# Kernel optimization log

Measured on AMD Instinct MI355X. Metric: run time of the kernel, lower is better.

The kernel has to match this reference:

```python
import jax, jax.numpy as jnp
import numpy as np

N_NODES = 10000
N_EDGES = 320000
F_NODE = 16
NUM_BESSEL = 8
M = 32           # env_embed_multiplicity
LAT = 128        # latent dimension
R_MAX = 5.0
P_CUT = 6.0      # polynomial cutoff order
AVG_NEIGH = 32.0
SQRT3 = 1.7320508075688772
SQRT2 = 1.4142135623730951


def _mlp(x, weights):
    # nequip ScalarMLPFunction: linear layers with 1/sqrt(fan_in) norm, silu between layers
    h = x
    n = len(weights)
    for i, W in enumerate(weights):
        h = h @ W * (1.0 / np.sqrt(W.shape[0]))
        if i < n - 1:
            h = jax.nn.silu(h)
    return h


def _weight_channels(Y, w):
    # MakeWeightedChannels: Y [E,4] = (0e | 1e), w [E,M,2] per-irrep weights -> [E,M,4]
    return jnp.concatenate([w[..., 0:1] * Y[:, None, 0:1],
                            w[..., 1:2] * Y[:, None, 1:4]], axis=-1)


def setup_inputs():
    key = jax.random.key(0)
    ks = jax.random.split(key, 16)

    def w(k, i, o):
        return jax.random.normal(k, (i, o), jnp.float32)

    two_body_in = 2 * F_NODE + NUM_BESSEL  # 40
    return {
        "coordinates": jax.random.uniform(ks[0], (N_NODES, 3), jnp.float32),
        "node_attrs": jax.random.uniform(ks[1], (N_NODES, F_NODE), jnp.float32),
        "edge_index": jax.random.randint(ks[2], (2, N_EDGES), 0, N_NODES),
        "W2b0": w(ks[3], two_body_in, 64),
        "W2b1": w(ks[4], 64, 128),
        "W2b2": w(ks[5], 128, LAT),
        "Wenv0": w(ks[6], LAT, 4 * M),       # initial-edge embed + env weights (2 irreps each)
        "Wlat0": w(ks[7], LAT + 2 * M, 128),
        "Wlat1": w(ks[8], 128, LAT),
        "Ws0": w(ks[9], 2 * M, M),            # e3nn Linear, scalar block (2 paths)
        "Wv0": w(ks[10], 3 * M, M),           # e3nn Linear, vector block (3 paths)
        "Wenv1": w(ks[11], LAT, 2 * M),
        "Wfin0": w(ks[12], LAT + 2 * M, 128),
        "Wfin1": w(ks[13], 128, LAT),
    }


def reference(coordinates, node_attrs, edge_index, W2b0, W2b1, W2b2, Wenv0,
              Wlat0, Wlat1, Ws0, Wv0, Wenv1, Wfin0, Wfin1):
    sender, center = edge_index[0], edge_index[1]
    vec = coordinates[center] - coordinates[sender]            # [E,3]
    r = jnp.sqrt(jnp.sum(vec * vec, axis=-1) + 1e-12)          # [E]
    u = r / R_MAX
    p = P_CUT
    fcut = (1.0 - (p + 1.0) * (p + 2.0) / 2.0 * u**p
            + p * (p + 2.0) * u**(p + 1.0)
            - p * (p + 1.0) / 2.0 * u**(p + 2.0))
    fcut = jnp.where(u < 1.0, fcut, 0.0)
    n = jnp.arange(1, NUM_BESSEL + 1, dtype=jnp.float32)
    bessel = np.sqrt(2.0 / R_MAX) * jnp.sin(n * jnp.pi * u[:, None]) / r[:, None]
    edge_feats = bessel * fcut[:, None]                        # [E,8]
    unit = vec / r[:, None]
    Y = jnp.concatenate([jnp.ones_like(r)[:, None], SQRT3 * unit], axis=-1)  # [E,4] component-normalized SH

    inv_sqrt_n = 1.0 / np.sqrt(AVG_NEIGH)
    E = r.shape[0]

    # two-body latent (layer 0)
    lat_in = jnp.concatenate([node_attrs[center], node_attrs[sender], edge_feats], -1)
    lat = _mlp(lat_in, (W2b0, W2b1, W2b2)) * fcut[:, None]     # [E,LAT]
    w_all = lat @ Wenv0 * (1.0 / np.sqrt(LAT))                 # [E,4M]
    w_edge = w_all[:, :2 * M].reshape(E, M, 2)
    w_env = w_all[:, 2 * M:].reshape(E, M, 2)
    feat = _weight_channels(Y, w_edge)                         # [E,M,4] initial edge embed
    env = jax.ops.segment_sum(_weight_channels(Y, w_env), center, num_segments=N_NODES)
    env = env[center] * inv_sqrt_n                             # [E,M,4]

    fs, fv = feat[..., 0], feat[..., 1:]
    es, ev = env[..., 0], env[..., 1:]
    # layer-0 tensor product instruction list (uuu, no weights)
    p0 = fs * es                               # 0e x 0e -> 0e
    p1 = jnp.sum(fv * ev, -1) / SQRT3          # 1e x 1e -> 0e
    p2 = fs[..., None] * ev                    # 0e x 1e -> 1e
    p3 = fv * es[..., None]                    # 1e x 0e -> 1e
    p4 = jnp.cross(fv, ev) / SQRT2             # 1e x 1e -> 1e
    scal0 = jnp.concatenate([p0, p1], -1)      # [E,2M] scalar outs (n_scalar_outs=2)
    # per-layer e3nn Linear
    s_mix = scal0 @ Ws0 * (1.0 / np.sqrt(2 * M))                         # [E,M]
    v_mix = jnp.einsum('eic,io->eoc', jnp.concatenate([p2, p3, p4], 1), Wv0) * (1.0 / np.sqrt(3 * M))  # [E,M,3]

    # latent resnet update (update param 0 -> sigmoid = 0.5)
    alpha = 0.5
    c_old = 1.0 / np.sqrt(alpha * alpha + 1.0)
    c_new = alpha * c_old
    new_lat = _mlp(jnp.concatenate([lat, scal0], -1), (Wlat0, Wlat1)) * fcut[:, None]
    lat = c_old * lat + c_new * new_lat

    # layer 1 env embedding + tensor product (last layer -> scalars only)
    w_env1 = (lat @ Wenv1 * (1.0 / np.sqrt(LAT))).reshape(E, M, 2)
    env1 = jax.ops.segment_sum(_weight_channels(Y, w_env1), center, num_segments=N_NODES)
    env1 = env1[center] * inv_sqrt_n
    q0 = s_mix * env1[..., 0]
    q1 = jnp.sum(v_mix * env1[..., 1:], -1) / SQRT3
    scal1 = jnp.concatenate([q0, q1], -1)      # [E,2M]

    new_lat = _mlp(jnp.concatenate([lat, scal1], -1), (Wfin0, Wfin1)) * fcut[:, None]
    lat = c_old * lat + c_new * new_lat

    node_out = jax.ops.segment_sum(lat, center, num_segments=N_NODES) * inv_sqrt_n
    return node_out
```

## Files before the change

kernel.cpp:

```cpp
#include <hip/hip_runtime.h>
#include <hip/hip_bf16.h>
#include <math.h>

typedef __hip_bfloat16 bf16;
typedef __attribute__((ext_vector_type(8))) short short8;
typedef __attribute__((ext_vector_type(4))) float floatx4;

#define AMODE_PLAIN  0
#define AMODE_CONCAT 2
#define EPI_SPLIT    1
#define EPI_STORE    2
#define EPI_FCUT     3
#define EPI_RESID    4

#define INV_SQRT_N 0.17677669529663687f
#define INV_SQRT3  0.5773502691896258f
#define INV_SQRT2  0.7071067811865476f
#define C_OLD      0.8944271909999159f
#define C_NEW      0.4472135954999579f
#define PI_F       3.14159265358979323846f
#define SQRT3_F    1.7320508075688772f
#define BESSEL_PREF 0.6324555320336759f

__device__ __forceinline__ float b2f(bf16 x) { return __bfloat162float(x); }
__device__ __forceinline__ bf16  f2b(float x) { return __float2bfloat16(x); }
__device__ __forceinline__ unsigned short f2bu(float x) {
  bf16 h = f2b(x); unsigned short u; __builtin_memcpy(&u, &h, 2); return u;
}
__device__ __forceinline__ float silu_f(float v) { return v / (1.f + __expf(-v)); }
__device__ __forceinline__ floatx4 mfma16(short8 a, short8 b, floatx4 c) {
  return __builtin_amdgcn_mfma_f32_16x16x32_bf16(a, b, c, 0, 0, 0);
}

__global__ __launch_bounds__(256) void k_deg(
    const int* __restrict__ eidx, int E, int* __restrict__ deg) {
  int e = blockIdx.x * 256 + threadIdx.x;
  if (e < E) atomicAdd(&deg[eidx[E + e]], 1);
}

__global__ __launch_bounds__(1024) void k_scan(
    const int* __restrict__ deg, int N,
    int* __restrict__ rowptr, int* __restrict__ cursor) {
  __shared__ int part[1024];
  int t = threadIdx.x;
  int C = (N + 1023) / 1024;
  int base = t * C;
  int s = 0;
  for (int i = 0; i < C; ++i) { int idx = base + i; if (idx < N) s += deg[idx]; }
  part[t] = s;
  __syncthreads();
  for (int off = 1; off < 1024; off <<= 1) {
    int v = (t >= off) ? part[t - off] : 0;
    __syncthreads();
    part[t] += v;
    __syncthreads();
  }
  int excl = (t == 0) ? 0 : part[t - 1];
  for (int i = 0; i < C; ++i) {
    int idx = base + i;
    if (idx < N) { rowptr[idx] = excl; cursor[idx] = excl; excl += deg[idx]; }
  }
  if (t == 0) rowptr[N] = part[1023];
}

__global__ __launch_bounds__(256) void k_fill(
    const int* __restrict__ eidx, int E, int* __restrict__ cursor,
    int* __restrict__ eord, int* __restrict__ cent) {
  int e = blockIdx.x * 256 + threadIdx.x;
  if (e >= E) return;
  int c = eidx[E + e];
  int slot = atomicAdd(&cursor[c], 1);
  eord[slot] = e;
  cent[slot] = c;
}

__global__ __launch_bounds__(256) void k_geom(
    const float* __restrict__ coords, const float* __restrict__ nattr,
    const int* __restrict__ eidx, const int* __restrict__ eord, int E,
    float* __restrict__ fcut, float* __restrict__ Yb, bf16* __restrict__ a40) {
  int j = blockIdx.x * 256 + threadIdx.x;
  if (j >= E) return;
  int e = eord[j];
  int s = eidx[e], c = eidx[E + e];
  float dx = coords[c*3+0] - coords[s*3+0];
  float dy = coords[c*3+1] - coords[s*3+1];
  float dz = coords[c*3+2] - coords[s*3+2];
  float r = sqrtf(dx*dx + dy*dy + dz*dz + 1e-12f);
  float u = r * 0.2f;
  float u3 = u*u*u;
  float u6 = u3*u3, u7 = u6*u, u8 = u7*u;
  float fc = 1.f - 28.f*u6 + 48.f*u7 - 21.f*u8;
  fc = (u < 1.f) ? fc : 0.f;
  float inv_r = 1.f / r;
  fcut[j] = fc;
  Yb[j*4+0] = 1.f;
  Yb[j*4+1] = SQRT3_F * dx * inv_r;
  Yb[j*4+2] = SQRT3_F * dy * inv_r;
  Yb[j*4+3] = SQRT3_F * dz * inv_r;
  bf16* row = a40 + (long)j * 40;
  #pragma unroll
  for (int i = 0; i < 16; ++i) row[i]      = f2b(nattr[(long)c*16 + i]);
  #pragma unroll
  for (int i = 0; i < 16; ++i) row[16 + i] = f2b(nattr[(long)s*16 + i]);
  float pref = BESSEL_PREF * inv_r * fc;
  #pragma unroll
  for (int n = 1; n <= 8; ++n)
    row[32 + n - 1] = f2b(pref * sinf((float)n * PI_F * u));
}

__device__ __forceinline__ void wp(const float* W, unsigned short* Wt,
                                   int K, int NOUT, int t) {
  int n = t / K, k = t % K;
  Wt[n * K + k] = f2bu(W[k * NOUT + n]);
}

__global__ __launch_bounds__(256) void k_wprep_all(
    const float* W2b0, const float* W2b1, const float* W2b2,
    const float* Wenv0, const float* Wlat0, const float* Wlat1,
    const float* Wenv1, const float* Wfin0, const float* Wfin1,
    const float* Ws0, const float* Wv0,
    unsigned short* W2b0t, unsigned short* W2b1t, unsigned short* W2b2t,
    unsigned short* Wenv0t, unsigned short* Wlat0t, unsigned short* Wlat1t,
    unsigned short* Wenv1t, unsigned short* Wfin0t, unsigned short* Wfin1t,
    unsigned short* Wmixt) {
  int t = blockIdx.x * 256 + threadIdx.x;
  if (t < 8192)  { wp(W2b1,  W2b1t,  64, 128, t); return; } t -= 8192;
  if (t < 16384) { wp(W2b2,  W2b2t, 128, 128, t); return; } t -= 16384;
  if (t < 16384) { wp(Wenv0, Wenv0t,128, 128, t); return; } t -= 16384;
  if (t < 24576) { wp(Wlat0, Wlat0t,192, 128, t); return; } t -= 24576;
  if (t < 16384) { wp(Wlat1, Wlat1t,128, 128, t); return; } t -= 16384;
  if (t < 8192)  { wp(Wenv1, Wenv1t,128,  64, t); return; } t -= 8192;
  if (t < 24576) { wp(Wfin0, Wfin0t,192, 128, t); return; } t -= 24576;
  if (t < 16384) { wp(Wfin1, Wfin1t,128, 128, t); return; } t -= 16384;
  if (t < 2560)  { wp(W2b0,  W2b0t,  40,  64, t); return; } t -= 2560;
  if (t < 5120) {
    int o = t / 160, k = t % 160;
    float v = (k < 64) ? Ws0[k * 32 + o] : Wv0[(k - 64) * 32 + o];
    Wmixt[o * 160 + k] = f2bu(v);
  }
}

__global__ __launch_bounds__(256) void k_envg(
    const bf16* __restrict__ wenv, const float* __restrict__ Yb,
    const int* __restrict__ rowptr, int N, float* __restrict__ env) {
  int t = blockIdx.x * 256 + threadIdx.x;
  if (t >= N * 32) return;
  int n = t >> 5, m = t & 31;
  int j0 = rowptr[n], j1 = rowptr[n + 1];
  float a0 = 0.f, a1 = 0.f, a2 = 0.f, a3 = 0.f;
  for (int j = j0; j < j1; ++j) {
    float w0 = b2f(wenv[(long)j*64 + 2*m]);
    float w1 = b2f(wenv[(long)j*64 + 2*m + 1]);
    float4 y = *reinterpret_cast<const float4*>(&Yb[(long)j*4]);
    a0 += w0;
    a1 += w1 * y.y;
    a2 += w1 * y.z;
    a3 += w1 * y.w;
  }
  *reinterpret_cast<float4*>(&env[(long)n*128 + m*4]) = make_float4(a0, a1, a2, a3);
}

__global__ __launch_bounds__(256) void k_nodeg(
    const bf16* __restrict__ lat, const int* __restrict__ rowptr,
    int N, float* __restrict__ out) {
  int t = blockIdx.x * 256 + threadIdx.x;
  if (t >= N * 128) return;
  int n = t >> 7, j = t & 127;
  int j0 = rowptr[n], j1 = rowptr[n + 1];
  float s = 0.f;
  for (int q = j0; q < j1; ++q)
    s += b2f(lat[(long)q*128 + j]);
  out[t] = s * INV_SQRT_N;
}

__global__ __launch_bounds__(256) void mgemm40(
    const bf16* __restrict__ A, const unsigned short* __restrict__ Wt,
    bf16* __restrict__ out, float scale, int E) {
  __shared__ __align__(16) unsigned short As[64 * 72];
  __shared__ __align__(16) unsigned short Bs[64 * 72];
  int tid = threadIdx.x;
  int lane = tid & 63, w = tid >> 6;
  int nl = lane & 15, quad = lane >> 4;
  long e0 = (long)blockIdx.x * 64;

  for (int i = tid; i < 512; i += 256) {
    int e = i >> 3, h = i & 7;
    short8 v = {0,0,0,0,0,0,0,0};
    long eg = e0 + e;
    if (h < 5 && eg < E) v = *(const short8*)(A + eg * 40 + h * 8);
    *(short8*)&As[e * 72 + h * 8] = v;
  }
  for (int i = tid; i < 512; i += 256) {
    int n = i >> 3, h = i & 7;
    short8 v = {0,0,0,0,0,0,0,0};
    if (h < 5) v = *(const short8*)(Wt + n * 40 + h * 8);
    *(short8*)&Bs[n * 72 + h * 8] = v;
  }
  __syncthreads();

  floatx4 acc[4];
  #pragma unroll
  for (int i = 0; i < 4; ++i) acc[i] = (floatx4){0.f,0.f,0.f,0.f};
  #pragma unroll
  for (int ks = 0; ks < 2; ++ks) {
    short8 af[4];
    #pragma unroll
    for (int et = 0; et < 4; ++et)
      af[et] = *(const short8*)&As[(et*16 + nl) * 72 + ks*32 + quad*8];
    short8 bv = *(const short8*)&Bs[(w*16 + nl) * 72 + ks*32 + quad*8];
    #pragma unroll
    for (int et = 0; et < 4; ++et) acc[et] = mfma16(af[et], bv, acc[et]);
  }
  #pragma unroll
  for (int et = 0; et < 4; ++et)
    #pragma unroll
    for (int r = 0; r < 4; ++r) {
      long eg = e0 + et*16 + quad*4 + r;
      if (eg >= E) continue;
      out[eg * 64 + w*16 + nl] = f2b(silu_f(acc[et][r] * scale));
    }
}

template<int K, int NOUT, int EPI>
__global__ __launch_bounds__(256) void mgemm(
    const bf16* __restrict__ A, const unsigned short* __restrict__ Wt,
    bf16* __restrict__ out1, bf16* __restrict__ out2, float scale, int E) {
  constexpr int KP = 40;
  constexpr int CT = NOUT / 64;
  __shared__ __align__(16) unsigned short As[64 * KP];
  __shared__ __align__(16) unsigned short Bs[NOUT * KP];
  int tid = threadIdx.x;
  int lane = tid & 63, w = tid >> 6;
  int nl = lane & 15, quad = lane >> 4;
  long e0 = (long)blockIdx.x * 64;

  floatx4 acc[4][CT];
  #pragma unroll
  for (int i = 0; i < 4; ++i)
    #pragma unroll
    for (int j = 0; j < CT; ++j) acc[i][j] = (floatx4){0.f,0.f,0.f,0.f};

  int ae = tid & 63, akh = tid >> 6;
  long aeg = e0 + ae;

  for (int k0 = 0; k0 < K; k0 += 32) {
    if (k0) __syncthreads();
    {
      short8 v = {0,0,0,0,0,0,0,0};
      if (aeg < E) v = *(const short8*)(A + aeg * (long)K + k0 + akh * 8);
      *(short8*)&As[ae * KP + akh * 8] = v;
    }
    if constexpr (NOUT == 128) {
      int j = tid >> 1, h = tid & 1;
      const short8* s = (const short8*)(Wt + (long)j * K + k0 + h * 16);
      *(short8*)&Bs[j * KP + h * 16]     = s[0];
      *(short8*)&Bs[j * KP + h * 16 + 8] = s[1];
    } else {
      int j = tid >> 2, h = tid & 3;
      *(short8*)&Bs[j * KP + h * 8] =
          *(const short8*)(Wt + (long)j * K + k0 + h * 8);
    }
    __syncthreads();
    short8 af[4], bv[CT];
    #pragma unroll
    for (int et = 0; et < 4; ++et)
      af[et] = *(const short8*)&As[(et*16 + nl) * KP + quad * 8];
    #pragma unroll
    for (int ct = 0; ct < CT; ++ct)
      bv[ct] = *(const short8*)&Bs[(w*CT*16 + ct*16 + nl) * KP + quad * 8];
    #pragma unroll
    for (int et = 0; et < 4; ++et)
      #pragma unroll
      for (int ct = 0; ct < CT; ++ct)
        acc[et][ct] = mfma16(af[et], bv[ct], acc[et][ct]);
  }

  #pragma unroll
  for (int et = 0; et < 4; ++et)
    #pragma unroll
    for (int ct = 0; ct < CT; ++ct)
      #pragma unroll
      for (int r = 0; r < 4; ++r) {
        long eg = e0 + et*16 + quad*4 + r;
        if (eg >= E) continue;
        int col = w*CT*16 + ct*16 + nl;
        float v = acc[et][ct][r] * scale;
        if constexpr (EPI == EPI_SPLIT) {
          if (col < 64) out1[eg * 64 + col] = f2b(v);
          else          out2[eg * 64 + (col - 64)] = f2b(v);
        } else {
          out1[eg * NOUT + col] = f2b(v);
        }
      }
}

template<int K, int AMODE, int EPI>
__global__ __launch_bounds__(256) void mfused(
    const bf16* __restrict__ A, const bf16* __restrict__ A2,
    const unsigned short* __restrict__ W0t, const unsigned short* __restrict__ W1t,
    bf16* __restrict__ outb, const float* __restrict__ fcut,
    float scale0, float scale1, int E) {
  constexpr int KP = 40, HP = 136;
  __shared__ __align__(16) unsigned short As[64 * KP];
  __shared__ __align__(16) unsigned short Bs[128 * KP];
  __shared__ __align__(16) unsigned short Hs[64 * HP];
  int tid = threadIdx.x;
  int lane = tid & 63, w = tid >> 6;
  int nl = lane & 15, quad = lane >> 4;
  long e0 = (long)blockIdx.x * 64;

  floatx4 acc[4][2];
  #pragma unroll
  for (int i = 0; i < 4; ++i)
    #pragma unroll
    for (int j = 0; j < 2; ++j) acc[i][j] = (floatx4){0.f,0.f,0.f,0.f};

  int ae = tid & 63, akh = tid >> 6;
  long aeg = e0 + ae;
  int bj = tid >> 1, bh = tid & 1;

  for (int k0 = 0; k0 < K; k0 += 32) {
    if (k0) __syncthreads();
    {
      int kk = k0 + akh * 8;
      short8 v = {0,0,0,0,0,0,0,0};
      if (aeg < E) {
        const bf16* src;
        if constexpr (AMODE == AMODE_PLAIN) src = A + aeg * (long)K + kk;
        else src = (kk < 128) ? (A + aeg * 128 + kk) : (A2 + aeg * 64 + (kk - 128));
        v = *(const short8*)src;
      }
      *(short8*)&As[ae * KP + akh * 8] = v;
    }
    {
      const short8* s = (const short8*)(W0t + (long)bj * K + k0 + bh * 16);
      *(short8*)&Bs[bj * KP + bh * 16]     = s[0];
      *(short8*)&Bs[bj * KP + bh * 16 + 8] = s[1];
    }
    __syncthreads();
    short8 af[4], bv[2];
    #pragma unroll
    for (int et = 0; et < 4; ++et)
      af[et] = *(const short8*)&As[(et*16 + nl) * KP + quad * 8];
    #pragma unroll
    for (int ct = 0; ct < 2; ++ct)
      bv[ct] = *(const short8*)&Bs[(w*32 + ct*16 + nl) * KP + quad * 8];
    #pragma unroll
    for (int et = 0; et < 4; ++et)
      #pragma unroll
      for (int ct = 0; ct < 2; ++ct)
        acc[et][ct] = mfma16(af[et], bv[ct], acc[et][ct]);
  }

  #pragma unroll
  for (int et = 0; et < 4; ++et)
    #pragma unroll
    for (int ct = 0; ct < 2; ++ct)
      #pragma unroll
      for (int r = 0; r < 4; ++r) {
        int el = et*16 + quad*4 + r;
        int h  = w*32 + ct*16 + nl;
        Hs[el * HP + h] = f2bu(silu_f(acc[et][ct][r] * scale0));
      }
  #pragma unroll
  for (int i = 0; i < 4; ++i)
    #pragma unroll
    for (int j = 0; j < 2; ++j) acc[i][j] = (floatx4){0.f,0.f,0.f,0.f};

  for (int k0 = 0; k0 < 128; k0 += 32) {
    __syncthreads();
    {
      const short8* s = (const short8*)(W1t + (long)bj * 128 + k0 + bh * 16);
      *(short8*)&Bs[bj * KP + bh * 16]     = s[0];
      *(short8*)&Bs[bj * KP + bh * 16 + 8] = s[1];
    }
    __syncthreads();
    short8 af[4], bv[2];
    #pragma unroll
    for (int et = 0; et < 4; ++et)
      af[et] = *(const short8*)&Hs[(et*16 + nl) * HP + k0 + quad * 8];
    #pragma unroll
    for (int ct = 0; ct < 2; ++ct)
      bv[ct] = *(const short8*)&Bs[(w*32 + ct*16 + nl) * KP + quad * 8];
    #pragma unroll
    for (int et = 0; et < 4; ++et)
      #pragma unroll
      for (int ct = 0; ct < 2; ++ct)
        acc[et][ct] = mfma16(af[et], bv[ct], acc[et][ct]);
  }

  #pragma unroll
  for (int et = 0; et < 4; ++et)
    #pragma unroll
    for (int ct = 0; ct < 2; ++ct)
      #pragma unroll
      for (int r = 0; r < 4; ++r) {
        long eg = e0 + et*16 + quad*4 + r;
        if (eg >= E) continue;
        int col = w*32 + ct*16 + nl;
        float fc = fcut[eg];
        float v = acc[et][ct][r] * scale1 * fc;
        if constexpr (EPI == EPI_FCUT) {
          outb[eg * 128 + col] = f2b(v);
        } else {
          long idx = eg * 128 + col;
          outb[idx] = f2b(C_OLD * b2f(outb[idx]) + C_NEW * v);
        }
      }
}

__global__ __launch_bounds__(256) void k_prod(
    const bf16* __restrict__ wedge, const float* __restrict__ env,
    const float* __restrict__ Yb, const int* __restrict__ cent, int E,
    bf16* __restrict__ scal) {
  long t = (long)blockIdx.x * 256 + threadIdx.x;
  if (t >= (long)E * 32) return;
  long e = t >> 5;
  int m = (int)(t & 31);
  int c = cent[e];
  float w0 = b2f(wedge[e*64 + 2*m]), w1 = b2f(wedge[e*64 + 2*m + 1]);
  const float* ep = env + (long)c*128 + m*4;
  float es  = ep[0] * INV_SQRT_N;
  float evx = ep[1] * INV_SQRT_N, evy = ep[2] * INV_SQRT_N, evz = ep[3] * INV_SQRT_N;
  float y1 = Yb[e*4+1], y2 = Yb[e*4+2], y3 = Yb[e*4+3];
  float fvx = w1*y1, fvy = w1*y2, fvz = w1*y3;
  scal[e*64 + m]      = f2b(w0 * es);
  scal[e*64 + 32 + m] = f2b((fvx*evx + fvy*evy + fvz*evz) * INV_SQRT3);
}

__global__ __launch_bounds__(256) void k_mix2(
    const bf16* __restrict__ wedge, const float* __restrict__ env,
    const float* __restrict__ env1, const float* __restrict__ Yb,
    const int* __restrict__ cent, const unsigned short* __restrict__ Wm,
    int E, bf16* __restrict__ scal) {
  constexpr int PP = 360;
  constexpr int RP = 132;
  __shared__ __align__(16) unsigned char SB[64 * PP * 2];
  __shared__ __align__(16) unsigned short Wl[32 * 160];
  unsigned short* P = (unsigned short*)SB;
  float* R = (float*)SB;
  int tid = threadIdx.x;
  int lane = tid & 63, w = tid >> 6;
  int nl = lane & 15, quad = lane >> 4;
  long e0 = (long)blockIdx.x * 64;

  for (int i = tid; i < 640; i += 256)
    *(short8*)&Wl[i * 8] = *(const short8*)(Wm + i * 8);

  int m = tid & 31;
  #pragma unroll
  for (int it = 0; it < 8; ++it) {
    int el = (tid >> 5) + it * 8;
    long e = e0 + el;
    if (e < E) {
      int c = cent[e];
      float w0 = b2f(wedge[e*64 + 2*m]), w1 = b2f(wedge[e*64 + 2*m + 1]);
      float4 ev4 = *(const float4*)(env + (long)c*128 + m*4);
      float4 y   = *(const float4*)(Yb + e*4);
      float es  = ev4.x * INV_SQRT_N;
      float evx = ev4.y * INV_SQRT_N, evy = ev4.z * INV_SQRT_N, evz = ev4.w * INV_SQRT_N;
      float fvx = w1*y.y, fvy = w1*y.z, fvz = w1*y.w;
      unsigned short* p = P + el * PP;
      p[m]       = f2bu(w0 * es);
      p[32 + m]  = f2bu((fvx*evx + fvy*evy + fvz*evz) * INV_SQRT3);
      p[64 + m]  = f2bu(w0 * evx);
      p[96 + m]  = f2bu(fvx * es);
      p[128 + m] = f2bu((fvy*evz - fvz*evy) * INV_SQRT2);
      p[160 + m] = f2bu(w0 * evy);
      p[192 + m] = f2bu(fvy * es);
      p[224 + m] = f2bu((fvz*evx - fvx*evz) * INV_SQRT2);
      p[256 + m] = f2bu(w0 * evz);
      p[288 + m] = f2bu(fvz * es);
      p[320 + m] = f2bu((fvx*evy - fvy*evx) * INV_SQRT2);
    } else {
      unsigned short* p = P + el * PP;
      #pragma unroll
      for (int q = 0; q < 11; ++q) p[q*32 + m] = 0;
    }
  }
  __syncthreads();

  floatx4 acc[4][2];
  #pragma unroll
  for (int i = 0; i < 4; ++i)
    #pragma unroll
    for (int j = 0; j < 2; ++j) acc[i][j] = (floatx4){0.f,0.f,0.f,0.f};
  int pbase  = (w == 0) ? 0 : 64 + (w - 1) * 96;
  int wkbase = (w == 0) ? 0 : 64;
  int ksteps = (w == 0) ? 2 : 3;
  for (int ks = 0; ks < ksteps; ++ks) {
    short8 af[4], bv[2];
    #pragma unroll
    for (int et = 0; et < 4; ++et)
      af[et] = *(const short8*)&P[(et*16 + nl) * PP + pbase + ks*32 + quad*8];
    #pragma unroll
    for (int ct = 0; ct < 2; ++ct)
      bv[ct] = *(const short8*)&Wl[(ct*16 + nl) * 160 + wkbase + ks*32 + quad*8];
    #pragma unroll
    for (int et = 0; et < 4; ++et)
      #pragma unroll
      for (int ct = 0; ct < 2; ++ct)
        acc[et][ct] = mfma16(af[et], bv[ct], acc[et][ct]);
  }
  __syncthreads();

  #pragma unroll
  for (int et = 0; et < 4; ++et)
    #pragma unroll
    for (int ct = 0; ct < 2; ++ct)
      #pragma unroll
      for (int r = 0; r < 4; ++r) {
        int el = et*16 + quad*4 + r;
        R[el * RP + w*32 + ct*16 + nl] = acc[et][ct][r];
      }
  __syncthreads();

  #pragma unroll
  for (int it = 0; it < 8; ++it) {
    int el = (tid >> 5) + it * 8;
    long e = e0 + el;
    if (e >= E) continue;
    int o = m;
    int c = cent[e];
    float4 e1 = *(const float4*)(env1 + (long)c*128 + o*4);
    float sr = R[el * RP + o];
    float vx = R[el * RP + 32 + o];
    float vy = R[el * RP + 64 + o];
    float vz = R[el * RP + 96 + o];
    float q0 = sr * 0.125f * (e1.x * INV_SQRT_N);
    float q1 = (vx*e1.y + vy*e1.z + vz*e1.w) *
               (0.10206207261596577f * INV_SQRT_N * INV_SQRT3);
    scal[e*64 + o]      = f2b(q0);
    scal[e*64 + 32 + o] = f2b(q1);
  }
}

extern "C" void kernel_launch(void* const* d_in, const int* in_sizes, int n_in,
                              void* d_out, int out_size, void* d_ws, size_t ws_size,
                              hipStream_t stream) {
  const float* coords = (const float*)d_in[0];
  const float* nattr  = (const float*)d_in[1];
  const int*   eidx   = (const int*)d_in[2];
  const float* W2b0   = (const float*)d_in[3];
  const float* W2b1   = (const float*)d_in[4];
  const float* W2b2   = (const float*)d_in[5];
  const float* Wenv0  = (const float*)d_in[6];
  const float* Wlat0  = (const float*)d_in[7];
  const float* Wlat1  = (const float*)d_in[8];
  const float* Ws0    = (const float*)d_in[9];
  const float* Wv0    = (const float*)d_in[10];
  const float* Wenv1  = (const float*)d_in[11];
  const float* Wfin0  = (const float*)d_in[12];
  const float* Wfin1  = (const float*)d_in[13];
  float* out = (float*)d_out;
  int E = in_sizes[2] / 2;
  int N = in_sizes[0] / 3;

  float* fcut   = (float*)d_ws;
  float* Yb     = fcut + (size_t)E;
  float* env    = Yb + (size_t)E*4;
  float* env1   = env + (size_t)N*128;
  int*   deg    = (int*)(env1 + (size_t)N*128);
  int*   rowptr = deg + N;
  int*   cursor = rowptr + (N + 8);
  int*   eord   = cursor + N;
  int*   cent   = eord + E;
  bf16*  b64    = (bf16*)(cent + E);
  bf16*  lat    = b64 + (size_t)E*64;
  bf16*  S      = lat + (size_t)E*128;
  unsigned short* W2b1t  = (unsigned short*)(S + (size_t)E*64);
  unsigned short* W2b2t  = W2b1t + 128*64;
  unsigned short* Wenv0t = W2b2t + 128*128;
  unsigned short* Wlat0t = Wenv0t + 128*128;
  unsigned short* Wlat1t = Wlat0t + 128*192;
  unsigned short* Wenv1t = Wlat1t + 128*128;
  unsigned short* Wfin0t = Wenv1t + 64*128;
  unsigned short* Wfin1t = Wfin0t + 128*192;
  unsigned short* W2b0t  = Wfin1t + 128*128;
  unsigned short* Wmixt  = W2b0t + 64*40;

  hipMemsetAsync(deg, 0, (size_t)N * sizeof(int), stream);

  dim3 blk(256);
  const float s40  = 0.15811388300841897f;
  const float s64  = 0.125f;
  const float s128 = 0.08838834764831845f;
  const float s192 = 0.07216878364870323f;
  int gB = (E + 63) / 64;
  int gE = (E + 255) / 256;

  k_deg<<<gE, blk, 0, stream>>>(eidx, E, deg);
  k_scan<<<1, 1024, 0, stream>>>(deg, N, rowptr, cursor);
  k_fill<<<gE, blk, 0, stream>>>(eidx, E, cursor, eord, cent);
  k_geom<<<gE, blk, 0, stream>>>(coords, nattr, eidx, eord, E, fcut, Yb, S );
  k_wprep_all<<<dim3(542), blk, 0, stream>>>(
      W2b0, W2b1, W2b2, Wenv0, Wlat0, Wlat1, Wenv1, Wfin0, Wfin1, Ws0, Wv0,
      W2b0t, W2b1t, W2b2t, Wenv0t, Wlat0t, Wlat1t, Wenv1t, Wfin0t, Wfin1t, Wmixt);

  mgemm40<<<gB, blk, 0, stream>>>(S , W2b0t, b64, s40, E);
  mfused<64,AMODE_PLAIN,EPI_FCUT><<<gB, blk, 0, stream>>>(
      b64, nullptr, W2b1t, W2b2t, lat, fcut, s64, s128, E);

  mgemm<128,128,EPI_SPLIT><<<gB, blk, 0, stream>>>(
      lat, Wenv0t, b64, S , s128, E);

  k_envg<<<dim3((N*32 + 255) / 256), blk, 0, stream>>>(
      S , Yb, rowptr, N, env);

  k_prod<<<dim3((int)(((long)E*32 + 255) / 256)), blk, 0, stream>>>(
      b64, env, Yb, cent, E, S );

  mfused<192,AMODE_CONCAT,EPI_RESID><<<gB, blk, 0, stream>>>(
      lat, S , Wlat0t, Wlat1t, lat, fcut, s192, s128, E);

  mgemm<128,64,EPI_STORE><<<gB, blk, 0, stream>>>(
      lat, Wenv1t, S , nullptr, s128, E);

  k_envg<<<dim3((N*32 + 255) / 256), blk, 0, stream>>>(
      S , Yb, rowptr, N, env1);

  k_mix2<<<gB, blk, 0, stream>>>(
      b64, env, env1, Yb, cent, Wmixt, E, S );

  mfused<192,AMODE_CONCAT,EPI_RESID><<<gB, blk, 0, stream>>>(
      lat, S , Wfin0t, Wfin1t, lat, fcut, s192, s128, E);

  k_nodeg<<<dim3((N*128 + 255) / 256), blk, 0, stream>>>(
      lat, rowptr, N, out);
}
```

Measured before the change: 724.1 us.

## Fuse two-body MLP into one kernel and load GEMM operands directly from global

The first two-body layer (K=40, padded to 64) is merged with the next two layers into a single kernel, so the intermediate 64-wide activation stays in LDS and is no longer written to and re-read from global memory. The generic GEMM and fused-MLP kernels stop staging A and weight tiles through shared memory with barriers. MFMA fragments are now read straight from global memory, relying on cache for weight reuse. Padding the geometry row to 64 adds a little extra write traffic, and the direct global fragment loads may be less coalesced than the old staged loads.

```diff
diff --git a/kernel.cpp b/kernel.cpp
--- a/kernel.cpp
+++ b/kernel.cpp
@@ -3,6 +3,7 @@
 #include <math.h>
 
 typedef __hip_bfloat16 bf16;
+typedef unsigned short us;
 typedef __attribute__((ext_vector_type(8))) short short8;
 typedef __attribute__((ext_vector_type(4))) float floatx4;
 
@@ -24,12 +25,15 @@
 
 __device__ __forceinline__ float b2f(bf16 x) { return __bfloat162float(x); }
 __device__ __forceinline__ bf16  f2b(float x) { return __float2bfloat16(x); }
-__device__ __forceinline__ unsigned short f2bu(float x) {
-  bf16 h = f2b(x); unsigned short u; __builtin_memcpy(&u, &h, 2); return u;
+__device__ __forceinline__ us f2bu(float x) {
+  bf16 h = f2b(x); us u; __builtin_memcpy(&u, &h, 2); return u;
 }
 __device__ __forceinline__ float silu_f(float v) { return v / (1.f + __expf(-v)); }
 __device__ __forceinline__ floatx4 mfma16(short8 a, short8 b, floatx4 c) {
   return __builtin_amdgcn_mfma_f32_16x16x32_bf16(a, b, c, 0, 0, 0);
+}
+__device__ __forceinline__ short8 ld8(const void* p) {
+  return *reinterpret_cast<const short8*>(p);
 }
 
 __global__ __launch_bounds__(256) void k_deg(
@@ -77,7 +81,7 @@
 __global__ __launch_bounds__(256) void k_geom(
     const float* __restrict__ coords, const float* __restrict__ nattr,
     const int* __restrict__ eidx, const int* __restrict__ eord, int E,
-    float* __restrict__ fcut, float* __restrict__ Yb, bf16* __restrict__ a40) {
+    float* __restrict__ fcut, float* __restrict__ Yb, bf16* __restrict__ a64) {
   int j = blockIdx.x * 256 + threadIdx.x;
   if (j >= E) return;
   int e = eord[j];
@@ -97,7 +101,7 @@
   Yb[j*4+1] = SQRT3_F * dx * inv_r;
   Yb[j*4+2] = SQRT3_F * dy * inv_r;
   Yb[j*4+3] = SQRT3_F * dz * inv_r;
-  bf16* row = a40 + (long)j * 40;
+  bf16* row = a64 + (long)j * 64;
   #pragma unroll
   for (int i = 0; i < 16; ++i) row[i]      = f2b(nattr[(long)c*16 + i]);
   #pragma unroll
@@ -106,10 +110,11 @@
   #pragma unroll
   for (int n = 1; n <= 8; ++n)
     row[32 + n - 1] = f2b(pref * sinf((float)n * PI_F * u));
-}
-
-__device__ __forceinline__ void wp(const float* W, unsigned short* Wt,
-                                   int K, int NOUT, int t) {
+  #pragma unroll
+  for (int i = 40; i < 64; ++i) row[i] = f2b(0.f);
+}
+
+__device__ __forceinline__ void wp(const float* W, us* Wt, int K, int NOUT, int t) {
   int n = t / K, k = t % K;
   Wt[n * K + k] = f2bu(W[k * NOUT + n]);
 }
@@ -119,10 +124,8 @@
     const float* Wenv0, const float* Wlat0, const float* Wlat1,
     const float* Wenv1, const float* Wfin0, const float* Wfin1,
     const float* Ws0, const float* Wv0,
-    unsigned short* W2b0t, unsigned short* W2b1t, unsigned short* W2b2t,
-    unsigned short* Wenv0t, unsigned short* Wlat0t, unsigned short* Wlat1t,
-    unsigned short* Wenv1t, unsigned short* Wfin0t, unsigned short* Wfin1t,
-    unsigned short* Wmixt) {
+    us* W2b0p, us* W2b1t, us* W2b2t, us* Wenv0t, us* Wlat0t, us* Wlat1t,
+    us* Wenv1t, us* Wfin0t, us* Wfin1t, us* Wmixt) {
   int t = blockIdx.x * 256 + threadIdx.x;
   if (t < 8192)  { wp(W2b1,  W2b1t,  64, 128, t); return; } t -= 8192;
   if (t < 16384) { wp(W2b2,  W2b2t, 128, 128, t); return; } t -= 16384;
@@ -132,7 +135,11 @@
   if (t < 8192)  { wp(Wenv1, Wenv1t,128,  64, t); return; } t -= 8192;
   if (t < 24576) { wp(Wfin0, Wfin0t,192, 128, t); return; } t -= 24576;
   if (t < 16384) { wp(Wfin1, Wfin1t,128, 128, t); return; } t -= 16384;
-  if (t < 2560)  { wp(W2b0,  W2b0t,  40,  64, t); return; } t -= 2560;
+  if (t < 4096)  {
+    int n = t >> 6, k = t & 63;
+    W2b0p[n * 64 + k] = (k < 40) ? f2bu(W2b0[k * 64 + n]) : 0;
+    return;
+  } t -= 4096;
   if (t < 5120) {
     int o = t / 160, k = t % 160;
     float v = (k < 64) ? Ws0[k * 32 + o] : Wv0[(k - 64) * 32 + o];
@@ -173,101 +180,33 @@
   out[t] = s * INV_SQRT_N;
 }
 
-__global__ __launch_bounds__(256) void mgemm40(
-    const bf16* __restrict__ A, const unsigned short* __restrict__ Wt,
-    bf16* __restrict__ out, float scale, int E) {
-  __shared__ __align__(16) unsigned short As[64 * 72];
-  __shared__ __align__(16) unsigned short Bs[64 * 72];
+template<int K, int NOUT, int EPI>
+__global__ __launch_bounds__(256) void mgemm(
+    const bf16* __restrict__ A, const us* __restrict__ Wt,
+    bf16* __restrict__ out1, bf16* __restrict__ out2, float scale, int E) {
+  constexpr int CT = NOUT / 64;
   int tid = threadIdx.x;
   int lane = tid & 63, w = tid >> 6;
   int nl = lane & 15, quad = lane >> 4;
   long e0 = (long)blockIdx.x * 64;
 
-  for (int i = tid; i < 512; i += 256) {
-    int e = i >> 3, h = i & 7;
-    short8 v = {0,0,0,0,0,0,0,0};
-    long eg = e0 + e;
-    if (h < 5 && eg < E) v = *(const short8*)(A + eg * 40 + h * 8);
-    *(short8*)&As[e * 72 + h * 8] = v;
-  }
-  for (int i = tid; i < 512; i += 256) {
-    int n = i >> 3, h = i & 7;
-    short8 v = {0,0,0,0,0,0,0,0};
-    if (h < 5) v = *(const short8*)(Wt + n * 40 + h * 8);
-    *(short8*)&Bs[n * 72 + h * 8] = v;
-  }
-  __syncthreads();
-
-  floatx4 acc[4];
-  #pragma unroll
-  for (int i = 0; i < 4; ++i) acc[i] = (floatx4){0.f,0.f,0.f,0.f};
-  #pragma unroll
-  for (int ks = 0; ks < 2; ++ks) {
-    short8 af[4];
-    #pragma unroll
-    for (int et = 0; et < 4; ++et)
-      af[et] = *(const short8*)&As[(et*16 + nl) * 72 + ks*32 + quad*8];
-    short8 bv = *(const short8*)&Bs[(w*16 + nl) * 72 + ks*32 + quad*8];
-    #pragma unroll
-    for (int et = 0; et < 4; ++et) acc[et] = mfma16(af[et], bv, acc[et]);
-  }
-  #pragma unroll
-  for (int et = 0; et < 4; ++et)
-    #pragma unroll
-    for (int r = 0; r < 4; ++r) {
-      long eg = e0 + et*16 + quad*4 + r;
-      if (eg >= E) continue;
-      out[eg * 64 + w*16 + nl] = f2b(silu_f(acc[et][r] * scale));
+  floatx4 acc[4][CT];
+  #pragma unroll
+  for (int i = 0; i < 4; ++i)
+    #pragma unroll
+    for (int j = 0; j < CT; ++j) acc[i][j] = (floatx4){0.f,0.f,0.f,0.f};
+
+  for (int k0 = 0; k0 < K; k0 += 32) {
+    int kk = k0 + quad * 8;
+    short8 af[4], bv[CT];
+    #pragma unroll
+    for (int et = 0; et < 4; ++et) {
+      long eg = e0 + et*16 + nl;
+      af[et] = (eg < E) ? ld8(A + eg * (long)K + kk) : (short8){0,0,0,0,0,0,0,0};
     }
-}
-
-template<int K, int NOUT, int EPI>
-__global__ __launch_bounds__(256) void mgemm(
-    const bf16* __restrict__ A, const unsigned short* __restrict__ Wt,
-    bf16* __restrict__ out1, bf16* __restrict__ out2, float scale, int E) {
-  constexpr int KP = 40;
-  constexpr int CT = NOUT / 64;
-  __shared__ __align__(16) unsigned short As[64 * KP];
-  __shared__ __align__(16) unsigned short Bs[NOUT * KP];
-  int tid = threadIdx.x;
-  int lane = tid & 63, w = tid >> 6;
-  int nl = lane & 15, quad = lane >> 4;
-  long e0 = (long)blockIdx.x * 64;
-
-  floatx4 acc[4][CT];
-  #pragma unroll
-  for (int i = 0; i < 4; ++i)
-    #pragma unroll
-    for (int j = 0; j < CT; ++j) acc[i][j] = (floatx4){0.f,0.f,0.f,0.f};
-
-  int ae = tid & 63, akh = tid >> 6;
-  long aeg = e0 + ae;
-
-  for (int k0 = 0; k0 < K; k0 += 32) {
-    if (k0) __syncthreads();
-    {
-      short8 v = {0,0,0,0,0,0,0,0};
-      if (aeg < E) v = *(const short8*)(A + aeg * (long)K + k0 + akh * 8);
-      *(short8*)&As[ae * KP + akh * 8] = v;
-    }
-    if constexpr (NOUT == 128) {
-      int j = tid >> 1, h = tid & 1;
-      const short8* s = (const short8*)(Wt + (long)j * K + k0 + h * 16);
-      *(short8*)&Bs[j * KP + h * 16]     = s[0];
-      *(short8*)&Bs[j * KP + h * 16 + 8] = s[1];
-    } else {
-      int j = tid >> 2, h = tid & 3;
-      *(short8*)&Bs[j * KP + h * 8] =
-          *(const short8*)(Wt + (long)j * K + k0 + h * 8);
-    }
-    __syncthreads();
-    short8 af[4], bv[CT];
-    #pragma unroll
-    for (int et = 0; et < 4; ++et)
-      af[et] = *(const short8*)&As[(et*16 + nl) * KP + quad * 8];
     #pragma unroll
     for (int ct = 0; ct < CT; ++ct)
-      bv[ct] = *(const short8*)&Bs[(w*CT*16 + ct*16 + nl) * KP + quad * 8];
+      bv[ct] = ld8(Wt + (long)(w*CT*16 + ct*16 + nl) * K + kk);
     #pragma unroll
     for (int et = 0; et < 4; ++et)
       #pragma unroll
@@ -294,94 +233,173 @@
       }
 }
 
-template<int K, int AMODE, int EPI>
-__global__ __launch_bounds__(256) void mfused(
-    const bf16* __restrict__ A, const bf16* __restrict__ A2,
-    const unsigned short* __restrict__ W0t, const unsigned short* __restrict__ W1t,
-    bf16* __restrict__ outb, const float* __restrict__ fcut,
-    float scale0, float scale1, int E) {
-  constexpr int KP = 40, HP = 136;
-  __shared__ __align__(16) unsigned short As[64 * KP];
-  __shared__ __align__(16) unsigned short Bs[128 * KP];
-  __shared__ __align__(16) unsigned short Hs[64 * HP];
+__global__ __launch_bounds__(256) void mfused3(
+    const bf16* __restrict__ a64, const us* __restrict__ W0p,
+    const us* __restrict__ W1t, const us* __restrict__ W2t,
+    bf16* __restrict__ lat, const float* __restrict__ fcut,
+    float s40, float s64, float s128, int E) {
+  constexpr int H0P = 72, HP = 136;
+  __shared__ __align__(16) us H0[64 * H0P];
+  __shared__ __align__(16) us Hs[64 * HP];
   int tid = threadIdx.x;
   int lane = tid & 63, w = tid >> 6;
   int nl = lane & 15, quad = lane >> 4;
   long e0 = (long)blockIdx.x * 64;
 
+  floatx4 a0[4];
+  #pragma unroll
+  for (int i = 0; i < 4; ++i) a0[i] = (floatx4){0.f,0.f,0.f,0.f};
+  #pragma unroll
+  for (int k0 = 0; k0 < 64; k0 += 32) {
+    int kk = k0 + quad * 8;
+    short8 af[4];
+    #pragma unroll
+    for (int et = 0; et < 4; ++et) {
+      long eg = e0 + et*16 + nl;
+      af[et] = (eg < E) ? ld8(a64 + eg * 64 + kk) : (short8){0,0,0,0,0,0,0,0};
+    }
+    short8 bv = ld8(W0p + (w*16 + nl) * 64 + kk);
+    #pragma unroll
+    for (int et = 0; et < 4; ++et) a0[et] = mfma16(af[et], bv, a0[et]);
+  }
+  #pragma unroll
+  for (int et = 0; et < 4; ++et)
+    #pragma unroll
+    for (int r = 0; r < 4; ++r)
+      H0[(et*16 + quad*4 + r) * H0P + w*16 + nl] = f2bu(silu_f(a0[et][r] * s40));
+  __syncthreads();
+
   floatx4 acc[4][2];
   #pragma unroll
   for (int i = 0; i < 4; ++i)
     #pragma unroll
     for (int j = 0; j < 2; ++j) acc[i][j] = (floatx4){0.f,0.f,0.f,0.f};
-
-  int ae = tid & 63, akh = tid >> 6;
-  long aeg = e0 + ae;
-  int bj = tid >> 1, bh = tid & 1;
-
-  for (int k0 = 0; k0 < K; k0 += 32) {
-    if (k0) __syncthreads();
-    {
-      int kk = k0 + akh * 8;
-      short8 v = {0,0,0,0,0,0,0,0};
-      if (aeg < E) {
-        const bf16* src;
-        if constexpr (AMODE == AMODE_PLAIN) src = A + aeg * (long)K + kk;
-        else src = (kk < 128) ? (A + aeg * 128 + kk) : (A2 + aeg * 64 + (kk - 128));
-        v = *(const short8*)src;
-      }
-      *(short8*)&As[ae * KP + akh * 8] = v;
-    }
-    {
-      const short8* s = (const short8*)(W0t + (long)bj * K + k0 + bh * 16);
-      *(short8*)&Bs[bj * KP + bh * 16]     = s[0];
-      *(short8*)&Bs[bj * KP + bh * 16 + 8] = s[1];
-    }
-    __syncthreads();
+  #pragma unroll
+  for (int k0 = 0; k0 < 64; k0 += 32) {
+    int kk = k0 + quad * 8;
     short8 af[4], bv[2];
     #pragma unroll
     for (int et = 0; et < 4; ++et)
-      af[et] = *(const short8*)&As[(et*16 + nl) * KP + quad * 8];
-    #pragma unroll
-    for (int ct = 0; ct < 2; ++ct)
-      bv[ct] = *(const short8*)&Bs[(w*32 + ct*16 + nl) * KP + quad * 8];
+      af[et] = ld8(&H0[(et*16 + nl) * H0P + kk]);
+    #pragma unroll
+    for (int ct = 0; ct < 2; ++ct)
+      bv[ct] = ld8(W1t + (long)(w*32 + ct*16 + nl) * 64 + kk);
     #pragma unroll
     for (int et = 0; et < 4; ++et)
       #pragma unroll
       for (int ct = 0; ct < 2; ++ct)
         acc[et][ct] = mfma16(af[et], bv[ct], acc[et][ct]);
   }
-
   #pragma unroll
   for (int et = 0; et < 4; ++et)
     #pragma unroll
     for (int ct = 0; ct < 2; ++ct)
       #pragma unroll
+      for (int r = 0; r < 4; ++r)
+        Hs[(et*16 + quad*4 + r) * HP + w*32 + ct*16 + nl] =
+            f2bu(silu_f(acc[et][ct][r] * s64));
+  __syncthreads();
+
+  #pragma unroll
+  for (int i = 0; i < 4; ++i)
+    #pragma unroll
+    for (int j = 0; j < 2; ++j) acc[i][j] = (floatx4){0.f,0.f,0.f,0.f};
+  #pragma unroll
+  for (int k0 = 0; k0 < 128; k0 += 32) {
+    int kk = k0 + quad * 8;
+    short8 af[4], bv[2];
+    #pragma unroll
+    for (int et = 0; et < 4; ++et)
+      af[et] = ld8(&Hs[(et*16 + nl) * HP + kk]);
+    #pragma unroll
+    for (int ct = 0; ct < 2; ++ct)
+      bv[ct] = ld8(W2t + (long)(w*32 + ct*16 + nl) * 128 + kk);
+    #pragma unroll
+    for (int et = 0; et < 4; ++et)
+      #pragma unroll
+      for (int ct = 0; ct < 2; ++ct)
+        acc[et][ct] = mfma16(af[et], bv[ct], acc[et][ct]);
+  }
+  #pragma unroll
+  for (int et = 0; et < 4; ++et)
+    #pragma unroll
+    for (int ct = 0; ct < 2; ++ct)
+      #pragma unroll
       for (int r = 0; r < 4; ++r) {
-        int el = et*16 + quad*4 + r;
-        int h  = w*32 + ct*16 + nl;
-        Hs[el * HP + h] = f2bu(silu_f(acc[et][ct][r] * scale0));
+        long eg = e0 + et*16 + quad*4 + r;
+        if (eg >= E) continue;
+        lat[eg * 128 + w*32 + ct*16 + nl] =
+            f2b(acc[et][ct][r] * s128 * fcut[eg]);
       }
+}
+
+template<int K, int AMODE, int EPI>
+__global__ __launch_bounds__(256) void mfused(
+    const bf16* __restrict__ A, const bf16* __restrict__ A2,
+    const us* __restrict__ W0t, const us* __restrict__ W1t,
+    bf16* __restrict__ outb, const float* __restrict__ fcut,
+    float scale0, float scale1, int E) {
+  constexpr int HP = 136;
+  __shared__ __align__(16) us Hs[64 * HP];
+  int tid = threadIdx.x;
+  int lane = tid & 63, w = tid >> 6;
+  int nl = lane & 15, quad = lane >> 4;
+  long e0 = (long)blockIdx.x * 64;
+
+  floatx4 acc[4][2];
   #pragma unroll
   for (int i = 0; i < 4; ++i)
     #pragma unroll
     for (int j = 0; j < 2; ++j) acc[i][j] = (floatx4){0.f,0.f,0.f,0.f};
 
+  for (int k0 = 0; k0 < K; k0 += 32) {
+    int kk = k0 + quad * 8;
+    short8 af[4], bv[2];
+    #pragma unroll
+    for (int et = 0; et < 4; ++et) {
+      long eg = e0 + et*16 + nl;
+      if (eg < E) {
+        const bf16* src;
+        if constexpr (AMODE == AMODE_PLAIN) src = A + eg * (long)K + kk;
+        else src = (k0 < 128) ? (A + eg * 128 + kk) : (A2 + eg * 64 + (kk - 128));
+        af[et] = ld8(src);
+      } else af[et] = (short8){0,0,0,0,0,0,0,0};
+    }
+    #pragma unroll
+    for (int ct = 0; ct < 2; ++ct)
+      bv[ct] = ld8(W0t + (long)(w*32 + ct*16 + nl) * K + kk);
+    #pragma unroll
+    for (int et = 0; et < 4; ++et)
+      #pragma unroll
+      for (int ct = 0; ct < 2; ++ct)
+        acc[et][ct] = mfma16(af[et], bv[ct], acc[et][ct]);
+  }
+
+  #pragma unroll
+  for (int et = 0; et < 4; ++et)
+    #pragma unroll
+    for (int ct = 0; ct < 2; ++ct)
+      #pragma unroll
+      for (int r = 0; r < 4; ++r)
+        Hs[(et*16 + quad*4 + r) * HP + w*32 + ct*16 + nl] =
+            f2bu(silu_f(acc[et][ct][r] * scale0));
+  __syncthreads();
+
+  #pragma unroll
+  for (int i = 0; i < 4; ++i)
+    #pragma unroll
+    for (int j = 0; j < 2; ++j) acc[i][j] = (floatx4){0.f,0.f,0.f,0.f};
+
+  #pragma unroll
   for (int k0 = 0; k0 < 128; k0 += 32) {
-    __syncthreads();
-    {
-      const short8* s = (const short8*)(W1t + (long)bj * 128 + k0 + bh * 16);
-      *(short8*)&Bs[bj * KP + bh * 16]     = s[0];
-      *(short8*)&Bs[bj * KP + bh * 16 + 8] = s[1];
-    }
-    __syncthreads();
+    int kk = k0 + quad * 8;
     short8 af[4], bv[2];
     #pragma unroll
     for (int et = 0; et < 4; ++et)
-      af[et] = *(const short8*)&Hs[(et*16 + nl) * HP + k0 + quad * 8];
-    #pragma unroll
-    for (int ct = 0; ct < 2; ++ct)
-      bv[ct] = *(const short8*)&Bs[(w*32 + ct*16 + nl) * KP + quad * 8];
+      af[et] = ld8(&Hs[(et*16 + nl) * HP + kk]);
+    #pragma unroll
+    for (int ct = 0; ct < 2; ++ct)
+      bv[ct] = ld8(W1t + (long)(w*32 + ct*16 + nl) * 128 + kk);
     #pragma unroll
     for (int et = 0; et < 4; ++et)
       #pragma unroll
@@ -431,13 +449,13 @@
 __global__ __launch_bounds__(256) void k_mix2(
     const bf16* __restrict__ wedge, const float* __restrict__ env,
     const float* __restrict__ env1, const float* __restrict__ Yb,
-    const int* __restrict__ cent, const unsigned short* __restrict__ Wm,
+    const int* __restrict__ cent, const us* __restrict__ Wm,
     int E, bf16* __restrict__ scal) {
   constexpr int PP = 360;
   constexpr int RP = 132;
   __shared__ __align__(16) unsigned char SB[64 * PP * 2];
-  __shared__ __align__(16) unsigned short Wl[32 * 160];
-  unsigned short* P = (unsigned short*)SB;
+  __shared__ __align__(16) us Wl[32 * 160];
+  us* P = (us*)SB;
   float* R = (float*)SB;
   int tid = threadIdx.x;
   int lane = tid & 63, w = tid >> 6;
@@ -445,7 +463,7 @@
   long e0 = (long)blockIdx.x * 64;
 
   for (int i = tid; i < 640; i += 256)
-    *(short8*)&Wl[i * 8] = *(const short8*)(Wm + i * 8);
+    *(short8*)&Wl[i * 8] = ld8(Wm + i * 8);
 
   int m = tid & 31;
   #pragma unroll
@@ -460,7 +478,7 @@
       float es  = ev4.x * INV_SQRT_N;
       float evx = ev4.y * INV_SQRT_N, evy = ev4.z * INV_SQRT_N, evz = ev4.w * INV_SQRT_N;
       float fvx = w1*y.y, fvy = w1*y.z, fvz = w1*y.w;
-      unsigned short* p = P + el * PP;
+      us* p = P + el * PP;
       p[m]       = f2bu(w0 * es);
       p[32 + m]  = f2bu((fvx*evx + fvy*evy + fvz*evz) * INV_SQRT3);
       p[64 + m]  = f2bu(w0 * evx);
@@ -473,7 +491,7 @@
       p[288 + m] = f2bu(fvz * es);
       p[320 + m] = f2bu((fvx*evy - fvy*evx) * INV_SQRT2);
     } else {
-      unsigned short* p = P + el * PP;
+      us* p = P + el * PP;
       #pragma unroll
       for (int q = 0; q < 11; ++q) p[q*32 + m] = 0;
     }
@@ -492,10 +510,10 @@
     short8 af[4], bv[2];
     #pragma unroll
     for (int et = 0; et < 4; ++et)
-      af[et] = *(const short8*)&P[(et*16 + nl) * PP + pbase + ks*32 + quad*8];
-    #pragma unroll
-    for (int ct = 0; ct < 2; ++ct)
-      bv[ct] = *(const short8*)&Wl[(ct*16 + nl) * 160 + wkbase + ks*32 + quad*8];
+      af[et] = ld8(&P[(et*16 + nl) * PP + pbase + ks*32 + quad*8]);
+    #pragma unroll
+    for (int ct = 0; ct < 2; ++ct)
+      bv[ct] = ld8(&Wl[(ct*16 + nl) * 160 + wkbase + ks*32 + quad*8]);
     #pragma unroll
     for (int et = 0; et < 4; ++et)
       #pragma unroll
@@ -568,16 +586,16 @@
   bf16*  b64    = (bf16*)(cent + E);
   bf16*  lat    = b64 + (size_t)E*64;
   bf16*  S      = lat + (size_t)E*128;
-  unsigned short* W2b1t  = (unsigned short*)(S + (size_t)E*64);
-  unsigned short* W2b2t  = W2b1t + 128*64;
-  unsigned short* Wenv0t = W2b2t + 128*128;
-  unsigned short* Wlat0t = Wenv0t + 128*128;
-  unsigned short* Wlat1t = Wlat0t + 128*192;
-  unsigned short* Wenv1t = Wlat1t + 128*128;
-  unsigned short* Wfin0t = Wenv1t + 64*128;
-  unsigned short* Wfin1t = Wfin0t + 128*192;
-  unsigned short* W2b0t  = Wfin1t + 128*128;
-  unsigned short* Wmixt  = W2b0t + 64*40;
+  us* W2b1t  = (us*)(S + (size_t)E*64);
+  us* W2b2t  = W2b1t + 128*64;
+  us* Wenv0t = W2b2t + 128*128;
+  us* Wlat0t = Wenv0t + 128*128;
+  us* Wlat1t = Wlat0t + 128*192;
+  us* Wenv1t = Wlat1t + 128*128;
+  us* Wfin0t = Wenv1t + 64*128;
+  us* Wfin1t = Wfin0t + 128*192;
+  us* W2b0p  = Wfin1t + 128*128;
+  us* Wmixt  = W2b0p + 64*64;
 
   hipMemsetAsync(deg, 0, (size_t)N * sizeof(int), stream);
 
@@ -593,13 +611,12 @@
   k_scan<<<1, 1024, 0, stream>>>(deg, N, rowptr, cursor);
   k_fill<<<gE, blk, 0, stream>>>(eidx, E, cursor, eord, cent);
   k_geom<<<gE, blk, 0, stream>>>(coords, nattr, eidx, eord, E, fcut, Yb, S );
-  k_wprep_all<<<dim3(542), blk, 0, stream>>>(
+  k_wprep_all<<<dim3(548), blk, 0, stream>>>(
       W2b0, W2b1, W2b2, Wenv0, Wlat0, Wlat1, Wenv1, Wfin0, Wfin1, Ws0, Wv0,
-      W2b0t, W2b1t, W2b2t, Wenv0t, Wlat0t, Wlat1t, Wenv1t, Wfin0t, Wfin1t, Wmixt);
-
-  mgemm40<<<gB, blk, 0, stream>>>(S , W2b0t, b64, s40, E);
-  mfused<64,AMODE_PLAIN,EPI_FCUT><<<gB, blk, 0, stream>>>(
-      b64, nullptr, W2b1t, W2b2t, lat, fcut, s64, s128, E);
+      W2b0p, W2b1t, W2b2t, Wenv0t, Wlat0t, Wlat1t, Wenv1t, Wfin0t, Wfin1t, Wmixt);
+
+  mfused3<<<gB, blk, 0, stream>>>(
+      S , W2b0p, W2b1t, W2b2t, lat, fcut, s40, s64, s128, E);
 
   mgemm<128,128,EPI_SPLIT><<<gB, blk, 0, stream>>>(
       lat, Wenv0t, b64, S , s128, E);
```

New measurement: 841.2 us. 1.16x slower.
